# Optimization experiments

Measured on AMD Instinct MI355X. Metric: run time of the kernel, lower is better.

Reference implementation:

```python
import jax, jax.numpy as jnp
import numpy as np

N = 1048576      # total rows across all sets
D = 128          # input_dim == output_dim
S = 4096         # number of segments (sets)


def setup_inputs() -> dict:
    key = jax.random.key(0)
    k1, k2, k3, k4, k5 = jax.random.split(key, 5)
    x = jax.random.normal(k1, (N, D), dtype=jnp.float32)
    # sorted segment ids emulate torch.split with variable lengths l
    seg_ids = jnp.sort(jax.random.randint(k2, (N,), 0, S, dtype=jnp.int32))
    Gamma_W = jax.random.normal(k3, (D, D), dtype=jnp.float32) * (1.0 / np.sqrt(D))
    Gamma_b = jax.random.normal(k4, (D,), dtype=jnp.float32) * 0.01
    Lambda_W = jax.random.normal(k5, (D, D), dtype=jnp.float32) * (1.0 / np.sqrt(D))
    return {"x": x, "seg_ids": seg_ids, "num_segments": S,
            "Gamma_W": Gamma_W, "Gamma_b": Gamma_b, "Lambda_W": Lambda_W}


def reference(x, seg_ids, num_segments, Gamma_W, Gamma_b, Lambda_W):
    # per-segment sum pooling (op(s, 0) over each split)  -> [S, D]
    xs = jax.ops.segment_sum(x, seg_ids, num_segments=num_segments,
                             indices_are_sorted=True)
    # Lambda: Linear without bias on pooled features      -> [S, D]
    xm = xs @ Lambda_W.T
    # Gamma: Linear with bias, minus repeat_interleave(xm, l) == xm[seg_ids]
    out = x @ Gamma_W.T + Gamma_b - xm[seg_ids]
    return out
```

## Files before the change

kernel.cpp:

```cpp
#include <hip/hip_runtime.h>

#define NROWS 1048576
#define D 128
#define S 4096

typedef __bf16 bf16;
typedef __attribute__((ext_vector_type(8))) __bf16 bf16x8;
typedef __attribute__((ext_vector_type(4))) __bf16 bf16x4;
typedef __attribute__((ext_vector_type(4))) float f32x4;

__global__ __launch_bounds__(256) void k_init(const float* __restrict__ GW,
                                              float* __restrict__ xs,
                                              bf16* __restrict__ gwb) {
    int i = blockIdx.x * 256 + threadIdx.x;
    if (i < S * D) xs[i] = 0.f;
    if (i < D * D) gwb[i] = (bf16)GW[i];
}

__global__ __launch_bounds__(256) void k_segsum(const float* __restrict__ x,
                                                const int* __restrict__ sid,
                                                float* __restrict__ xs) {
    __shared__ int ssid[256];
    const int t = threadIdx.x;
    const size_t r0 = (size_t)blockIdx.x * 256;
    ssid[t] = sid[r0 + t];
    __syncthreads();
    const int col = t & 127;
    const int st  = t >> 7;
    float acc = 0.f;
    int cur = ssid[st];
    for (int i = 0; i < 128; i += 4) {
        float v[4];
        int   s[4];
#pragma unroll
        for (int u = 0; u < 4; ++u) {
            int rl = 2 * (i + u) + st;
            v[u] = x[(r0 + rl) * D + col];
            s[u] = ssid[rl];
        }
#pragma unroll
        for (int u = 0; u < 4; ++u) {
            if (s[u] != cur) {
                atomicAdd(&xs[(size_t)cur * D + col], acc);
                acc = 0.f;
                cur = s[u];
            }
            acc += v[u];
        }
    }
    atomicAdd(&xs[(size_t)cur * D + col], acc);
}

#define SEGS_PER_BLOCK 8
__global__ __launch_bounds__(128) void k_lambda(const float* __restrict__ xs,
                                                const float* __restrict__ LW,
                                                const float* __restrict__ gb,
                                                float* __restrict__ v) {
    __shared__ float L[128 * 129];
    __shared__ float xrow[128];
    const int t = threadIdx.x;
    for (int i = 0; i < 128; ++i)
        L[i * 129 + t] = LW[i * 128 + t];
    const float bj = gb[t];
    for (int sl = 0; sl < SEGS_PER_BLOCK; ++sl) {
        const int s = blockIdx.x * SEGS_PER_BLOCK + sl;
        __syncthreads();
        xrow[t] = xs[(size_t)s * D + t];
        __syncthreads();
        float acc = 0.f;
#pragma unroll 8
        for (int k = 0; k < 128; ++k)
            acc += xrow[k] * L[t * 129 + k];
        v[(size_t)s * D + t] = bj - acc;
    }
}

__global__ __launch_bounds__(256) void k_main(const float* __restrict__ x,
                                              const int* __restrict__ sid,
                                              const bf16* __restrict__ gwb,
                                              const float* __restrict__ v,
                                              float* __restrict__ out) {
    __shared__ bf16 As[128 * 136];
    __shared__ bf16 Bs[128 * 136];
    __shared__ int  ssid[128];
    const int t = threadIdx.x;
    const size_t r0 = (size_t)blockIdx.x * 128;

    if (t < 128) ssid[t] = sid[r0 + t];

#pragma unroll
    for (int i = 0; i < 8; ++i) {
        int idx = i * 256 + t;
        int row = idx >> 4;
        int k8  = idx & 15;
        bf16x8 val = *(const bf16x8*)(gwb + (size_t)idx * 8);
        *(bf16x8*)&Bs[row * 136 + k8 * 8] = val;
    }

#pragma unroll
    for (int i = 0; i < 16; ++i) {
        int idx = i * 256 + t;
        int row = idx >> 5;
        int c4  = idx & 31;
        float4 xv = *(const float4*)(x + r0 * D + (size_t)idx * 4);
        bf16x4 bv;
        bv[0] = (bf16)xv.x; bv[1] = (bf16)xv.y; bv[2] = (bf16)xv.z; bv[3] = (bf16)xv.w;
        *(bf16x4*)&As[row * 136 + c4 * 4] = bv;
    }
    __syncthreads();

    const int wave = t >> 6, lane = t & 63;
    const int wm = (wave >> 1) * 64;
    const int wn = (wave & 1) * 64;
    const int lm = lane & 15, quad = lane >> 4;

    f32x4 acc[4][4];
#pragma unroll
    for (int mi = 0; mi < 4; ++mi)
#pragma unroll
        for (int ni = 0; ni < 4; ++ni)
            acc[mi][ni] = (f32x4){0.f, 0.f, 0.f, 0.f};

#pragma unroll
    for (int kb = 0; kb < 128; kb += 32) {
        bf16x8 af[4], bb[4];
#pragma unroll
        for (int mi = 0; mi < 4; ++mi)
            af[mi] = *(const bf16x8*)&As[(wm + mi * 16 + lm) * 136 + kb + quad * 8];
#pragma unroll
        for (int ni = 0; ni < 4; ++ni)
            bb[ni] = *(const bf16x8*)&Bs[(wn + ni * 16 + lm) * 136 + kb + quad * 8];
#pragma unroll
        for (int mi = 0; mi < 4; ++mi)
#pragma unroll
            for (int ni = 0; ni < 4; ++ni)
                acc[mi][ni] = __builtin_amdgcn_mfma_f32_16x16x32_bf16(
                    af[mi], bb[ni], acc[mi][ni], 0, 0, 0);
    }

#pragma unroll
    for (int mi = 0; mi < 4; ++mi) {
        const int rbase = wm + mi * 16 + quad * 4;
#pragma unroll
        for (int reg = 0; reg < 4; ++reg) {
            const int rl = rbase + reg;
            const int s = ssid[rl];
            const float* vrow = v + (size_t)s * D;
            const size_t obase = (r0 + rl) * D;
#pragma unroll
            for (int ni = 0; ni < 4; ++ni) {
                const int j = wn + ni * 16 + lm;
                out[obase + j] = acc[mi][ni][reg] + vrow[j];
            }
        }
    }
}

extern "C" void kernel_launch(void* const* d_in, const int* in_sizes, int n_in,
                              void* d_out, int out_size, void* d_ws, size_t ws_size,
                              hipStream_t stream) {
    const float* x   = (const float*)d_in[0];
    const int*   sid = (const int*)d_in[1];
    const float* GW  = (const float*)d_in[3];
    const float* gb  = (const float*)d_in[4];
    const float* LW  = (const float*)d_in[5];
    float* out = (float*)d_out;

    float* xs  = (float*)d_ws;
    float* v   = xs + S * D;
    bf16*  gwb = (bf16*)(v + S * D);

    k_init  <<<(S * D + 255) / 256, 256, 0, stream>>>(GW, xs, gwb);
    k_segsum<<<NROWS / 256,          256, 0, stream>>>(x, sid, xs);
    k_lambda<<<S / SEGS_PER_BLOCK,   128, 0, stream>>>(xs, LW, gb, v);
    k_main  <<<NROWS / 128,          256, 0, stream>>>(x, sid, gwb, v, out);
}
```

Baseline: 977.0 us.

## Vectorize segsum loads, drop B smem tile, add nontemporal hints and occupancy bound

The segment-sum kernel now has each thread load float4 vectors with nontemporal hints and covers 512 rows per block, so the block count falls and each thread issues wider loads. The main GEMM kernel no longer stages the bf16 Gamma weights in shared memory; it reads B fragments straight from global memory, which halves LDS use and allows a launch bound of 3 blocks per CU. The x loads and output stores are marked nontemporal to cut cache pollution. The risks are four scalar atomics per segment boundary in segsum, and repeated uncoalesced global reads of the weights, which rely on L1/L2 hits.

```diff
diff --git a/kernel.cpp b/kernel.cpp
--- a/kernel.cpp
+++ b/kernel.cpp
@@ -17,38 +17,47 @@
     if (i < D * D) gwb[i] = (bf16)GW[i];
 }
 
+#define RPB 512
 __global__ __launch_bounds__(256) void k_segsum(const float* __restrict__ x,
                                                 const int* __restrict__ sid,
                                                 float* __restrict__ xs) {
-    __shared__ int ssid[256];
+    __shared__ int ssid[RPB];
     const int t = threadIdx.x;
-    const size_t r0 = (size_t)blockIdx.x * 256;
-    ssid[t] = sid[r0 + t];
+    const size_t r0 = (size_t)blockIdx.x * RPB;
+    ssid[t]       = sid[r0 + t];
+    ssid[t + 256] = sid[r0 + t + 256];
     __syncthreads();
-    const int col = t & 127;
-    const int st  = t >> 7;
-    float acc = 0.f;
+    const int c4 = (t & 31) * 4;
+    const int st = t >> 5;
+    f32x4 acc = {0.f, 0.f, 0.f, 0.f};
     int cur = ssid[st];
-    for (int i = 0; i < 128; i += 4) {
-        float v[4];
+    for (int i = 0; i < 64; i += 4) {
+        f32x4 v[4];
         int   s[4];
 #pragma unroll
         for (int u = 0; u < 4; ++u) {
-            int rl = 2 * (i + u) + st;
-            v[u] = x[(r0 + rl) * D + col];
+            int rl = (i + u) * 8 + st;
+            v[u] = __builtin_nontemporal_load(
+                       (const f32x4*)(x + (r0 + rl) * D + c4));
             s[u] = ssid[rl];
         }
 #pragma unroll
         for (int u = 0; u < 4; ++u) {
             if (s[u] != cur) {
-                atomicAdd(&xs[(size_t)cur * D + col], acc);
-                acc = 0.f;
+                atomicAdd(&xs[(size_t)cur * D + c4 + 0], acc[0]);
+                atomicAdd(&xs[(size_t)cur * D + c4 + 1], acc[1]);
+                atomicAdd(&xs[(size_t)cur * D + c4 + 2], acc[2]);
+                atomicAdd(&xs[(size_t)cur * D + c4 + 3], acc[3]);
+                acc = (f32x4){0.f, 0.f, 0.f, 0.f};
                 cur = s[u];
             }
             acc += v[u];
         }
     }
-    atomicAdd(&xs[(size_t)cur * D + col], acc);
+    atomicAdd(&xs[(size_t)cur * D + c4 + 0], acc[0]);
+    atomicAdd(&xs[(size_t)cur * D + c4 + 1], acc[1]);
+    atomicAdd(&xs[(size_t)cur * D + c4 + 2], acc[2]);
+    atomicAdd(&xs[(size_t)cur * D + c4 + 3], acc[3]);
 }
 
 #define SEGS_PER_BLOCK 8
@@ -75,13 +84,12 @@
     }
 }
 
-__global__ __launch_bounds__(256) void k_main(const float* __restrict__ x,
-                                              const int* __restrict__ sid,
-                                              const bf16* __restrict__ gwb,
-                                              const float* __restrict__ v,
-                                              float* __restrict__ out) {
+__global__ __launch_bounds__(256, 3) void k_main(const float* __restrict__ x,
+                                                 const int* __restrict__ sid,
+                                                 const bf16* __restrict__ gwb,
+                                                 const float* __restrict__ v,
+                                                 float* __restrict__ out) {
     __shared__ bf16 As[128 * 136];
-    __shared__ bf16 Bs[128 * 136];
     __shared__ int  ssid[128];
     const int t = threadIdx.x;
     const size_t r0 = (size_t)blockIdx.x * 128;
@@ -89,22 +97,14 @@
     if (t < 128) ssid[t] = sid[r0 + t];
 
 #pragma unroll
-    for (int i = 0; i < 8; ++i) {
-        int idx = i * 256 + t;
-        int row = idx >> 4;
-        int k8  = idx & 15;
-        bf16x8 val = *(const bf16x8*)(gwb + (size_t)idx * 8);
-        *(bf16x8*)&Bs[row * 136 + k8 * 8] = val;
-    }
-
-#pragma unroll
     for (int i = 0; i < 16; ++i) {
         int idx = i * 256 + t;
         int row = idx >> 5;
         int c4  = idx & 31;
-        float4 xv = *(const float4*)(x + r0 * D + (size_t)idx * 4);
+        f32x4 xv = __builtin_nontemporal_load(
+                       (const f32x4*)(x + r0 * D + (size_t)idx * 4));
         bf16x4 bv;
-        bv[0] = (bf16)xv.x; bv[1] = (bf16)xv.y; bv[2] = (bf16)xv.z; bv[3] = (bf16)xv.w;
+        bv[0] = (bf16)xv[0]; bv[1] = (bf16)xv[1]; bv[2] = (bf16)xv[2]; bv[3] = (bf16)xv[3];
         *(bf16x4*)&As[row * 136 + c4 * 4] = bv;
     }
     __syncthreads();
@@ -125,11 +125,12 @@
     for (int kb = 0; kb < 128; kb += 32) {
         bf16x8 af[4], bb[4];
 #pragma unroll
+        for (int ni = 0; ni < 4; ++ni)
+            bb[ni] = *(const bf16x8*)(gwb + (size_t)(wn + ni * 16 + lm) * 128
+                                          + kb + quad * 8);
+#pragma unroll
         for (int mi = 0; mi < 4; ++mi)
             af[mi] = *(const bf16x8*)&As[(wm + mi * 16 + lm) * 136 + kb + quad * 8];
-#pragma unroll
-        for (int ni = 0; ni < 4; ++ni)
-            bb[ni] = *(const bf16x8*)&Bs[(wn + ni * 16 + lm) * 136 + kb + quad * 8];
 #pragma unroll
         for (int mi = 0; mi < 4; ++mi)
 #pragma unroll
@@ -150,7 +151,8 @@
 #pragma unroll
             for (int ni = 0; ni < 4; ++ni) {
                 const int j = wn + ni * 16 + lm;
-                out[obase + j] = acc[mi][ni][reg] + vrow[j];
+                __builtin_nontemporal_store(acc[mi][ni][reg] + vrow[j],
+                                            &out[obase + j]);
             }
         }
     }
@@ -171,7 +173,7 @@
     bf16*  gwb = (bf16*)(v + S * D);
 
     k_init  <<<(S * D + 255) / 256, 256, 0, stream>>>(GW, xs, gwb);
-    k_segsum<<<NROWS / 256,          256, 0, stream>>>(x, sid, xs);
+    k_segsum<<<NROWS / RPB,          256, 0, stream>>>(x, sid, xs);
     k_lambda<<<S / SEGS_PER_BLOCK,   128, 0, stream>>>(xs, LW, gb, v);
     k_main  <<<NROWS / 128,          256, 0, stream>>>(x, sid, gwb, v, out);
 }
```

After: 1.025 ms. 1.05x slower.
